# Kernel optimization log

Hardware: AMD Instinct MI355X
Metric: run time of the kernel (lower is better)

## Reference

```python
import jax, jax.numpy as jnp
import numpy as np

N_EMBED = 384
HEAD_SIZE = 64
B, T = 128, 512


def rope(x):
    # Faithful to source: fres = 1/1000**(arange(0,dim,2)//dim) -> integer
    # floor-div makes the exponent all zeros, so fres == 1 everywhere.
    Bx, Tx, D = x.shape
    half = D // 2
    fres = jnp.ones((half,), dtype=jnp.float32)
    ang = jnp.arange(Tx, dtype=jnp.float32)[:, None] * fres[None, :]  # (T, half)
    cos, sin = jnp.cos(ang), jnp.sin(ang)
    xr = x.reshape(Bx, Tx, half, 2)
    xe, xo = xr[..., 0], xr[..., 1]
    oe = xe * cos - xo * sin
    oo = xe * sin + xo * cos
    return jnp.stack([oe, oo], axis=-1).reshape(Bx, Tx, D)


def setup_inputs() -> dict:
    key = jax.random.key(0)
    ks = jax.random.split(key, 7)
    s = 1.0 / np.sqrt(N_EMBED)
    return {
        "x": jax.random.normal(ks[0], (B, T, N_EMBED), dtype=jnp.float32),
        "wq": jax.random.uniform(ks[1], (N_EMBED, HEAD_SIZE), jnp.float32, -s, s),
        "bq": jax.random.uniform(ks[2], (HEAD_SIZE,), jnp.float32, -s, s),
        "wk": jax.random.uniform(ks[3], (N_EMBED, HEAD_SIZE), jnp.float32, -s, s),
        "bk": jax.random.uniform(ks[4], (HEAD_SIZE,), jnp.float32, -s, s),
        "wv": jax.random.uniform(ks[5], (N_EMBED, HEAD_SIZE), jnp.float32, -s, s),
        "bv": jax.random.uniform(ks[6], (HEAD_SIZE,), jnp.float32, -s, s),
    }


def reference(x, wq, bq, wk, bk, wv, bv):
    Bx, Tx, C = x.shape  # C = n_embed; scale uses C per the source (not head_size)
    q = rope(x @ wq + bq)
    k = rope(x @ wk + bk)
    wei = jnp.einsum("bqd,bkd->bqk", q, k) * (C ** -0.5)  # (B, T, T)
    causal = jnp.tril(jnp.ones((Tx, Tx), dtype=bool))
    wei = jnp.where(causal, wei, -jnp.inf)
    wei = jax.nn.softmax(wei, axis=-1)
    v = x @ wv + bv
    return jnp.einsum("bqk,bkd->bqd", wei, v)
```

## Files before the change

kernel.cpp:

```cpp
#include <hip/hip_runtime.h>

#define TSEQ 512
#define NB   128
#define CDIM 384
#define HD   64
#define QSCALE 0.051031036307982884f
#define MBIAS  8.0f

typedef _Float16 half8  __attribute__((ext_vector_type(8)));
typedef _Float16 half4  __attribute__((ext_vector_type(4)));
typedef float    floatx4 __attribute__((ext_vector_type(4)));

__global__ void prep_w(const float* __restrict__ wq, const float* __restrict__ wk,
                       const float* __restrict__ wv, _Float16* __restrict__ Wt)
{
    int i = blockIdx.x * 256 + threadIdx.x;
    const int per = CDIM * HD;
    if (i >= 3 * per) return;
    int mat = i / per;
    int rem = i - mat * per;
    int k = rem / HD;
    int n = rem - k * HD;
    const float* w = (mat == 0) ? wq : ((mat == 1) ? wk : wv);
    Wt[((size_t)mat * HD + n) * CDIM + k] = (_Float16)w[rem];
}

__global__ __launch_bounds__(256) void qkv_gemm(
    const float* __restrict__ x, const _Float16* __restrict__ Wt,
    const float* __restrict__ bq, const float* __restrict__ bk,
    const float* __restrict__ bv,
    _Float16* __restrict__ Qw, _Float16* __restrict__ Kw,
    _Float16* __restrict__ Vtw, int b0)
{
    const int tid  = threadIdx.x;
    const int wave = tid >> 6;
    const int lane = tid & 63;
    const int l16  = lane & 15;
    const int quad = lane >> 4;

    const int row0 = blockIdx.x * 64;

    const float* xp = x + ((size_t)(b0 * TSEQ + row0) + l16) * CDIM + quad * 8;
    const _Float16* wp = Wt + (size_t)(wave * 16 + l16) * CDIM + quad * 8;

    floatx4 acc[12];
#pragma unroll
    for (int i = 0; i < 12; ++i)
#pragma unroll
        for (int r = 0; r < 4; ++r) acc[i][r] = 0.f;

    floatx4 ar[4][2];
    half8   br[3];
#pragma unroll
    for (int rt = 0; rt < 4; ++rt) {
        const float* p = xp + (size_t)rt * 16 * CDIM;
        ar[rt][0] = *(const floatx4*)p;
        ar[rt][1] = *(const floatx4*)(p + 4);
    }
#pragma unroll
    for (int m = 0; m < 3; ++m)
        br[m] = *(const half8*)(wp + (size_t)m * 64 * CDIM);

#pragma unroll
    for (int s = 0; s < 12; ++s) {
        floatx4 nr[4][2];
        half8   nb[3];
        if (s < 11) {
            const int kn = (s + 1) * 32;
#pragma unroll
            for (int rt = 0; rt < 4; ++rt) {
                const float* p = xp + (size_t)rt * 16 * CDIM + kn;
                nr[rt][0] = *(const floatx4*)p;
                nr[rt][1] = *(const floatx4*)(p + 4);
            }
#pragma unroll
            for (int m = 0; m < 3; ++m)
                nb[m] = *(const half8*)(wp + (size_t)m * 64 * CDIM + kn);
        }
        half8 a[4];
#pragma unroll
        for (int rt = 0; rt < 4; ++rt)
#pragma unroll
            for (int jj = 0; jj < 8; ++jj)
                a[rt][jj] = (_Float16)(jj < 4 ? ar[rt][0][jj] : ar[rt][1][jj - 4]);
#pragma unroll
        for (int m = 0; m < 3; ++m)
#pragma unroll
            for (int rt = 0; rt < 4; ++rt)
                acc[m * 4 + rt] =
                    __builtin_amdgcn_mfma_f32_16x16x32_f16(a[rt], br[m], acc[m * 4 + rt], 0, 0, 0);
        if (s < 11) {
#pragma unroll
            for (int rt = 0; rt < 4; ++rt) { ar[rt][0] = nr[rt][0]; ar[rt][1] = nr[rt][1]; }
#pragma unroll
            for (int m = 0; m < 3; ++m) br[m] = nb[m];
        }
    }

    const int c = wave * 16 + l16;
    const float bqv = bq[c], bkv = bk[c], bvv = bv[c];
    const int bidx = row0 >> 9;
    const int t00  = row0 & (TSEQ - 1);

#pragma unroll
    for (int rt = 0; rt < 4; ++rt) {
        half4 vpack;
#pragma unroll
        for (int r = 0; r < 4; ++r) {
            const int tr = t00 + rt * 16 + quad * 4 + r;
            const float st = sinf((float)tr);
            const float ct = cosf((float)tr);
            const int row = row0 + rt * 16 + quad * 4 + r;
            float vq = acc[rt][r] + bqv;
            float pq = __shfl_xor(vq, 1);
            vq = (c & 1) ? (pq * st + vq * ct) : (vq * ct - pq * st);
            Qw[(size_t)row * HD + c] = (_Float16)(vq * QSCALE);
            float vk = acc[4 + rt][r] + bkv;
            float pk = __shfl_xor(vk, 1);
            vk = (c & 1) ? (pk * st + vk * ct) : (vk * ct - pk * st);
            Kw[(size_t)row * HD + c] = (_Float16)vk;
            vpack[r] = (_Float16)(acc[8 + rt][r] + bvv);
        }
        const int tl0 = t00 + rt * 16 + quad * 4;
        *(half4*)(Vtw + ((size_t)bidx * HD + c) * TSEQ + tl0) = vpack;
    }
}

__global__ __launch_bounds__(256) void attn_kernel(
    const _Float16* __restrict__ Qw, const _Float16* __restrict__ Kw,
    const _Float16* __restrict__ Vtw, float* __restrict__ out, int b0)
{
    const int bl   = blockIdx.x;
    const int qt   = blockIdx.y;
    const int tid  = threadIdx.x;
    const int wave = tid >> 6;
    const int lane = tid & 63;
    const int l16  = lane & 15;
    const int quad = lane >> 4;

    __shared__ __align__(16) _Float16 pbuf[4][16][72];

    const _Float16* Qb = Qw  + (size_t)bl * TSEQ * HD;
    const _Float16* Kb = Kw  + (size_t)bl * TSEQ * HD;
    const _Float16* Vb = Vtw + (size_t)bl * HD * TSEQ;

    const int qr0 = qt * 64 + wave * 16;

    half8 aQ0 = *(const half8*)(Qb + (size_t)(qr0 + l16) * HD + quad * 8);
    half8 aQ1 = *(const half8*)(Qb + (size_t)(qr0 + l16) * HD + 32 + quad * 8);

    half8 ones;
#pragma unroll
    for (int jj = 0; jj < 8; ++jj) ones[jj] = (_Float16)1.f;

    floatx4 accO[4], accL;
#pragma unroll
    for (int s4 = 0; s4 < 4; ++s4)
#pragma unroll
        for (int r = 0; r < 4; ++r) accO[s4][r] = 0.f;
#pragma unroll
    for (int r = 0; r < 4; ++r) accL[r] = 0.f;

    for (int j = 0; j <= qt; ++j) {
        const int kb = j * 64;

        floatx4 st4[4];
#pragma unroll
        for (int s4 = 0; s4 < 4; ++s4) {
#pragma unroll
            for (int r = 0; r < 4; ++r) st4[s4][r] = 0.f;
            const _Float16* kp = Kb + (size_t)(kb + s4 * 16 + l16) * HD + quad * 8;
            half8 bK0 = *(const half8*)(kp);
            half8 bK1 = *(const half8*)(kp + 32);
            st4[s4] = __builtin_amdgcn_mfma_f32_16x16x32_f16(bK0, aQ0, st4[s4], 0, 0, 0);
            st4[s4] = __builtin_amdgcn_mfma_f32_16x16x32_f16(bK1, aQ1, st4[s4], 0, 0, 0);
        }

        half8 bV0[4], bV1[4];
#pragma unroll
        for (int s4 = 0; s4 < 4; ++s4) {
            const _Float16* vp = Vb + (size_t)(s4 * 16 + l16) * TSEQ + kb + quad * 8;
            bV0[s4] = *(const half8*)(vp);
            bV1[s4] = *(const half8*)(vp + 32);
        }

        const int qrow = qr0 + l16;
        if (j == qt) {
#pragma unroll
            for (int s4 = 0; s4 < 4; ++s4) {
                half4 w;
#pragma unroll
                for (int r = 0; r < 4; ++r) {
                    const int kcol = kb + s4 * 16 + quad * 4 + r;
                    float p = __expf(fminf(st4[s4][r], 18.f) - MBIAS);
                    w[r] = (_Float16)((kcol > qrow) ? 0.f : p);
                }
                *(half4*)(&pbuf[wave][l16][s4 * 16 + quad * 4]) = w;
            }
        } else {
#pragma unroll
            for (int s4 = 0; s4 < 4; ++s4) {
                half4 w;
#pragma unroll
                for (int r = 0; r < 4; ++r)
                    w[r] = (_Float16)__expf(fminf(st4[s4][r], 18.f) - MBIAS);
                *(half4*)(&pbuf[wave][l16][s4 * 16 + quad * 4]) = w;
            }
        }

        half8 aP0 = *(const half8*)(&pbuf[wave][l16][quad * 8]);
        half8 aP1 = *(const half8*)(&pbuf[wave][l16][32 + quad * 8]);

#pragma unroll
        for (int s4 = 0; s4 < 4; ++s4) {
            accO[s4] = __builtin_amdgcn_mfma_f32_16x16x32_f16(aP0, bV0[s4], accO[s4], 0, 0, 0);
            accO[s4] = __builtin_amdgcn_mfma_f32_16x16x32_f16(aP1, bV1[s4], accO[s4], 0, 0, 0);
        }
        accL = __builtin_amdgcn_mfma_f32_16x16x32_f16(aP0, ones, accL, 0, 0, 0);
        accL = __builtin_amdgcn_mfma_f32_16x16x32_f16(aP1, ones, accL, 0, 0, 0);
    }

    float inv[4];
#pragma unroll
    for (int r = 0; r < 4; ++r) inv[r] = 1.f / accL[r];
#pragma unroll
    for (int s4 = 0; s4 < 4; ++s4) {
        const int dcol = s4 * 16 + l16;
#pragma unroll
        for (int r = 0; r < 4; ++r) {
            const int qr = qr0 + quad * 4 + r;
            out[((size_t)(b0 + bl) * TSEQ + qr) * HD + dcol] = accO[s4][r] * inv[r];
        }
    }
}

extern "C" void kernel_launch(void* const* d_in, const int* in_sizes, int n_in,
                              void* d_out, int out_size, void* d_ws, size_t ws_size,
                              hipStream_t stream)
{
    char* ws = (char*)d_ws;
    _Float16* Wt = (_Float16*)ws;
    char* qkv_base = ws + 147456;

    const size_t per_b = (size_t)3 * TSEQ * HD * sizeof(_Float16);
    size_t avail = (ws_size > (size_t)147456) ? ws_size - 147456 : per_b;
    int nbc = (int)(avail / per_b);
    if (nbc > NB) nbc = NB;
    if (nbc < 1)  nbc = 1;

    const size_t chunk_elems = (size_t)nbc * TSEQ * HD;
    _Float16* Qw  = (_Float16*)qkv_base;
    _Float16* Kw  = Qw + chunk_elems;
    _Float16* Vtw = Kw + chunk_elems;

    prep_w<<<dim3((3 * CDIM * HD + 255) / 256), dim3(256), 0, stream>>>(
        (const float*)d_in[1], (const float*)d_in[3], (const float*)d_in[5], Wt);

    for (int b0 = 0; b0 < NB; b0 += nbc) {
        const int nb = (NB - b0 < nbc) ? (NB - b0) : nbc;
        qkv_gemm<<<dim3(nb * 8), dim3(256), 0, stream>>>(
            (const float*)d_in[0], Wt, (const float*)d_in[2], (const float*)d_in[4],
            (const float*)d_in[6], Qw, Kw, Vtw, b0);
        attn_kernel<<<dim3(nb, 8), dim3(256), 0, stream>>>(
            Qw, Kw, Vtw, (float*)d_out, b0);
    }
}
```

Before: 255.2 us.

## Stage QKV GEMM tiles in LDS and share K/V loads across two query tiles

```diff
diff --git a/kernel.cpp b/kernel.cpp
--- a/kernel.cpp
+++ b/kernel.cpp
@@ -10,6 +10,13 @@
 typedef _Float16 half8  __attribute__((ext_vector_type(8)));
 typedef _Float16 half4  __attribute__((ext_vector_type(4)));
 typedef float    floatx4 __attribute__((ext_vector_type(4)));
+
+typedef __attribute__((address_space(3))) unsigned int lds_u32;
+typedef const __attribute__((address_space(1))) unsigned int g_u32;
+
+__device__ __forceinline__ void load_lds16(const void* g, void* l) {
+    __builtin_amdgcn_global_load_lds((g_u32*)g, (lds_u32*)l, 16, 0, 0);
+}
 
 __global__ void prep_w(const float* __restrict__ wq, const float* __restrict__ wk,
                        const float* __restrict__ wv, _Float16* __restrict__ Wt)
@@ -32,6 +39,9 @@
     _Float16* __restrict__ Qw, _Float16* __restrict__ Kw,
     _Float16* __restrict__ Vtw, int b0)
 {
+    __shared__ __align__(16) float    xs[8 * 64 * 8];
+    __shared__ __align__(16) _Float16 wsb[8 * 192 * 8];
+
     const int tid  = threadIdx.x;
     const int wave = tid >> 6;
     const int lane = tid & 63;
@@ -39,9 +49,7 @@
     const int quad = lane >> 4;
 
     const int row0 = blockIdx.x * 64;
-
-    const float* xp = x + ((size_t)(b0 * TSEQ + row0) + l16) * CDIM + quad * 8;
-    const _Float16* wp = Wt + (size_t)(wave * 16 + l16) * CDIM + quad * 8;
+    const size_t rowg = (size_t)b0 * TSEQ + row0;
 
     floatx4 acc[12];
 #pragma unroll
@@ -49,80 +57,86 @@
 #pragma unroll
         for (int r = 0; r < 4; ++r) acc[i][r] = 0.f;
 
-    floatx4 ar[4][2];
-    half8   br[3];
-#pragma unroll
-    for (int rt = 0; rt < 4; ++rt) {
-        const float* p = xp + (size_t)rt * 16 * CDIM;
-        ar[rt][0] = *(const floatx4*)p;
-        ar[rt][1] = *(const floatx4*)(p + 4);
-    }
-#pragma unroll
-    for (int m = 0; m < 3; ++m)
-        br[m] = *(const half8*)(wp + (size_t)m * 64 * CDIM);
-
-#pragma unroll
-    for (int s = 0; s < 12; ++s) {
-        floatx4 nr[4][2];
-        half8   nb[3];
-        if (s < 11) {
-            const int kn = (s + 1) * 32;
-#pragma unroll
-            for (int rt = 0; rt < 4; ++rt) {
-                const float* p = xp + (size_t)rt * 16 * CDIM + kn;
-                nr[rt][0] = *(const floatx4*)p;
-                nr[rt][1] = *(const floatx4*)(p + 4);
-            }
-#pragma unroll
-            for (int m = 0; m < 3; ++m)
-                nb[m] = *(const half8*)(wp + (size_t)m * 64 * CDIM + kn);
-        }
-        half8 a[4];
-#pragma unroll
-        for (int rt = 0; rt < 4; ++rt)
+    for (int c = 0; c < 6; ++c) {
+        const int kk0 = c * 64;
+
+#pragma unroll
+        for (int i = 0; i < 4; ++i) {
+            const int I    = wave * 4 + i;
+            const int cell = I * 32 + (lane >> 1);
+            const int kblk = cell >> 6;
+            const int m    = cell & 63;
+            const int kin0 = (lane & 1) * 4;
+            const float* src = x + (rowg + m) * CDIM + kk0 + kblk * 8 + kin0;
+            load_lds16(src, (char*)xs + I * 1024);
+        }
+#pragma unroll
+        for (int i = 0; i < 6; ++i) {
+            const int I2   = wave * 6 + i;
+            const int c2   = I2 * 64 + lane;
+            const int kblk = c2 / 192;
+            const int n    = c2 - kblk * 192;
+            const _Float16* src = Wt + (size_t)n * CDIM + kk0 + kblk * 8;
+            load_lds16(src, (char*)wsb + I2 * 1024);
+        }
+        __syncthreads();
+
+#pragma unroll
+        for (int kb2 = 0; kb2 < 2; ++kb2) {
+            const int kblk = kb2 * 4 + quad;
+            const float* ap = xs + ((size_t)kblk * 64 + wave * 16 + l16) * 8;
+            floatx4 a0 = *(const floatx4*)ap;
+            floatx4 a1 = *(const floatx4*)(ap + 4);
+            half8 a;
 #pragma unroll
             for (int jj = 0; jj < 8; ++jj)
-                a[rt][jj] = (_Float16)(jj < 4 ? ar[rt][0][jj] : ar[rt][1][jj - 4]);
-#pragma unroll
-        for (int m = 0; m < 3; ++m)
-#pragma unroll
-            for (int rt = 0; rt < 4; ++rt)
-                acc[m * 4 + rt] =
-                    __builtin_amdgcn_mfma_f32_16x16x32_f16(a[rt], br[m], acc[m * 4 + rt], 0, 0, 0);
-        if (s < 11) {
-#pragma unroll
-            for (int rt = 0; rt < 4; ++rt) { ar[rt][0] = nr[rt][0]; ar[rt][1] = nr[rt][1]; }
-#pragma unroll
-            for (int m = 0; m < 3; ++m) br[m] = nb[m];
-        }
-    }
-
-    const int c = wave * 16 + l16;
-    const float bqv = bq[c], bkv = bk[c], bvv = bv[c];
+                a[jj] = (_Float16)(jj < 4 ? a0[jj] : a1[jj - 4]);
+            const _Float16* bp = wsb + ((size_t)kblk * 192 + l16) * 8;
+#pragma unroll
+            for (int i = 0; i < 12; ++i) {
+                half8 bb = *(const half8*)(bp + i * 128);
+                acc[i] = __builtin_amdgcn_mfma_f32_16x16x32_f16(a, bb, acc[i], 0, 0, 0);
+            }
+        }
+        __syncthreads();
+    }
+
+    float bq4[4], bk4[4], bv4[4];
+#pragma unroll
+    for (int s4 = 0; s4 < 4; ++s4) {
+        const int cc = s4 * 16 + l16;
+        bq4[s4] = bq[cc]; bk4[s4] = bk[cc]; bv4[s4] = bv[cc];
+    }
+    const int t00  = (row0 & (TSEQ - 1)) + wave * 16 + quad * 4;
     const int bidx = row0 >> 9;
-    const int t00  = row0 & (TSEQ - 1);
-
-#pragma unroll
-    for (int rt = 0; rt < 4; ++rt) {
+    const int rowb = row0 + wave * 16 + quad * 4;
+
+#pragma unroll
+    for (int r = 0; r < 4; ++r) {
+        const int t = t00 + r;
+        const float st = sinf((float)t);
+        const float ct = cosf((float)t);
+        const int row = rowb + r;
+#pragma unroll
+        for (int s4 = 0; s4 < 4; ++s4) {
+            const int cc = s4 * 16 + l16;
+            float vq = acc[s4][r] + bq4[s4];
+            float pq = __shfl_xor(vq, 1);
+            vq = (cc & 1) ? (pq * st + vq * ct) : (vq * ct - pq * st);
+            Qw[(size_t)row * HD + cc] = (_Float16)(vq * QSCALE);
+            float vk = acc[4 + s4][r] + bk4[s4];
+            float pk = __shfl_xor(vk, 1);
+            vk = (cc & 1) ? (pk * st + vk * ct) : (vk * ct - pk * st);
+            Kw[(size_t)row * HD + cc] = (_Float16)vk;
+        }
+    }
+#pragma unroll
+    for (int s4 = 0; s4 < 4; ++s4) {
+        const int cc = s4 * 16 + l16;
         half4 vpack;
 #pragma unroll
-        for (int r = 0; r < 4; ++r) {
-            const int tr = t00 + rt * 16 + quad * 4 + r;
-            const float st = sinf((float)tr);
-            const float ct = cosf((float)tr);
-            const int row = row0 + rt * 16 + quad * 4 + r;
-            float vq = acc[rt][r] + bqv;
-            float pq = __shfl_xor(vq, 1);
-            vq = (c & 1) ? (pq * st + vq * ct) : (vq * ct - pq * st);
-            Qw[(size_t)row * HD + c] = (_Float16)(vq * QSCALE);
-            float vk = acc[4 + rt][r] + bkv;
-            float pk = __shfl_xor(vk, 1);
-            vk = (c & 1) ? (pk * st + vk * ct) : (vk * ct - pk * st);
-            Kw[(size_t)row * HD + c] = (_Float16)vk;
-            vpack[r] = (_Float16)(acc[8 + rt][r] + bvv);
-        }
-        const int tl0 = t00 + rt * 16 + quad * 4;
-        *(half4*)(Vtw + ((size_t)bidx * HD + c) * TSEQ + tl0) = vpack;
+        for (int r = 0; r < 4; ++r) vpack[r] = (_Float16)(acc[8 + s4][r] + bv4[s4]);
+        *(half4*)(Vtw + ((size_t)bidx * HD + cc) * TSEQ + t00) = vpack;
     }
 }
 
@@ -130,8 +144,8 @@
     const _Float16* __restrict__ Qw, const _Float16* __restrict__ Kw,
     const _Float16* __restrict__ Vtw, float* __restrict__ out, int b0)
 {
-    const int bl   = blockIdx.x;
-    const int qt   = blockIdx.y;
+    const int qt   = blockIdx.x;
+    const int bl   = blockIdx.y;
     const int tid  = threadIdx.x;
     const int wave = tid >> 6;
     const int lane = tid & 63;
@@ -144,92 +158,129 @@
     const _Float16* Kb = Kw  + (size_t)bl * TSEQ * HD;
     const _Float16* Vb = Vtw + (size_t)bl * HD * TSEQ;
 
-    const int qr0 = qt * 64 + wave * 16;
-
-    half8 aQ0 = *(const half8*)(Qb + (size_t)(qr0 + l16) * HD + quad * 8);
-    half8 aQ1 = *(const half8*)(Qb + (size_t)(qr0 + l16) * HD + 32 + quad * 8);
+    const int qA = qt * 128 + wave * 16;
+    const int qB = qA + 64;
+    const int jd = 2 * qt;
+
+    half8 aQA0 = *(const half8*)(Qb + (size_t)(qA + l16) * HD + quad * 8);
+    half8 aQA1 = *(const half8*)(Qb + (size_t)(qA + l16) * HD + 32 + quad * 8);
+    half8 aQB0 = *(const half8*)(Qb + (size_t)(qB + l16) * HD + quad * 8);
+    half8 aQB1 = *(const half8*)(Qb + (size_t)(qB + l16) * HD + 32 + quad * 8);
 
     half8 ones;
 #pragma unroll
     for (int jj = 0; jj < 8; ++jj) ones[jj] = (_Float16)1.f;
 
-    floatx4 accO[4], accL;
-#pragma unroll
-    for (int s4 = 0; s4 < 4; ++s4)
-#pragma unroll
-        for (int r = 0; r < 4; ++r) accO[s4][r] = 0.f;
-#pragma unroll
-    for (int r = 0; r < 4; ++r) accL[r] = 0.f;
-
-    for (int j = 0; j <= qt; ++j) {
+    floatx4 accO[8], accL[2];
+#pragma unroll
+    for (int i = 0; i < 8; ++i)
+#pragma unroll
+        for (int r = 0; r < 4; ++r) accO[i][r] = 0.f;
+#pragma unroll
+    for (int s = 0; s < 2; ++s)
+#pragma unroll
+        for (int r = 0; r < 4; ++r) accL[s][r] = 0.f;
+
+    for (int j = 0; j <= jd + 1; ++j) {
         const int kb = j * 64;
 
-        floatx4 st4[4];
+        half8 bK0[4], bK1[4], bV0[4], bV1[4];
 #pragma unroll
         for (int s4 = 0; s4 < 4; ++s4) {
-#pragma unroll
-            for (int r = 0; r < 4; ++r) st4[s4][r] = 0.f;
             const _Float16* kp = Kb + (size_t)(kb + s4 * 16 + l16) * HD + quad * 8;
-            half8 bK0 = *(const half8*)(kp);
-            half8 bK1 = *(const half8*)(kp + 32);
-            st4[s4] = __builtin_amdgcn_mfma_f32_16x16x32_f16(bK0, aQ0, st4[s4], 0, 0, 0);
-            st4[s4] = __builtin_amdgcn_mfma_f32_16x16x32_f16(bK1, aQ1, st4[s4], 0, 0, 0);
-        }
-
-        half8 bV0[4], bV1[4];
-#pragma unroll
-        for (int s4 = 0; s4 < 4; ++s4) {
+            bK0[s4] = *(const half8*)(kp);
+            bK1[s4] = *(const half8*)(kp + 32);
             const _Float16* vp = Vb + (size_t)(s4 * 16 + l16) * TSEQ + kb + quad * 8;
             bV0[s4] = *(const half8*)(vp);
             bV1[s4] = *(const half8*)(vp + 32);
         }
 
-        const int qrow = qr0 + l16;
-        if (j == qt) {
+        if (j <= jd) {
+            floatx4 st4[4];
+#pragma unroll
+            for (int s4 = 0; s4 < 4; ++s4) {
+#pragma unroll
+                for (int r = 0; r < 4; ++r) st4[s4][r] = 0.f;
+                st4[s4] = __builtin_amdgcn_mfma_f32_16x16x32_f16(bK0[s4], aQA0, st4[s4], 0, 0, 0);
+                st4[s4] = __builtin_amdgcn_mfma_f32_16x16x32_f16(bK1[s4], aQA1, st4[s4], 0, 0, 0);
+            }
+            const int qrow = qA + l16;
 #pragma unroll
             for (int s4 = 0; s4 < 4; ++s4) {
                 half4 w;
 #pragma unroll
                 for (int r = 0; r < 4; ++r) {
-                    const int kcol = kb + s4 * 16 + quad * 4 + r;
                     float p = __expf(fminf(st4[s4][r], 18.f) - MBIAS);
-                    w[r] = (_Float16)((kcol > qrow) ? 0.f : p);
+                    if (j == jd) {
+                        const int kcol = kb + s4 * 16 + quad * 4 + r;
+                        if (kcol > qrow) p = 0.f;
+                    }
+                    w[r] = (_Float16)p;
                 }
                 *(half4*)(&pbuf[wave][l16][s4 * 16 + quad * 4]) = w;
             }
-        } else {
+            half8 aP0 = *(const half8*)(&pbuf[wave][l16][quad * 8]);
+            half8 aP1 = *(const half8*)(&pbuf[wave][l16][32 + quad * 8]);
+#pragma unroll
+            for (int s4 = 0; s4 < 4; ++s4) {
+                accO[s4] = __builtin_amdgcn_mfma_f32_16x16x32_f16(aP0, bV0[s4], accO[s4], 0, 0, 0);
+                accO[s4] = __builtin_amdgcn_mfma_f32_16x16x32_f16(aP1, bV1[s4], accO[s4], 0, 0, 0);
+            }
+            accL[0] = __builtin_amdgcn_mfma_f32_16x16x32_f16(aP0, ones, accL[0], 0, 0, 0);
+            accL[0] = __builtin_amdgcn_mfma_f32_16x16x32_f16(aP1, ones, accL[0], 0, 0, 0);
+        }
+
+        {
+            floatx4 st4[4];
+#pragma unroll
+            for (int s4 = 0; s4 < 4; ++s4) {
+#pragma unroll
+                for (int r = 0; r < 4; ++r) st4[s4][r] = 0.f;
+                st4[s4] = __builtin_amdgcn_mfma_f32_16x16x32_f16(bK0[s4], aQB0, st4[s4], 0, 0, 0);
+                st4[s4] = __builtin_amdgcn_mfma_f32_16x16x32_f16(bK1[s4], aQB1, st4[s4], 0, 0, 0);
+            }
+            const int qrow = qB + l16;
 #pragma unroll
             for (int s4 = 0; s4 < 4; ++s4) {
                 half4 w;
 #pragma unroll
-                for (int r = 0; r < 4; ++r)
-                    w[r] = (_Float16)__expf(fminf(st4[s4][r], 18.f) - MBIAS);
+                for (int r = 0; r < 4; ++r) {
+                    float p = __expf(fminf(st4[s4][r], 18.f) - MBIAS);
+                    if (j == jd + 1) {
+                        const int kcol = kb + s4 * 16 + quad * 4 + r;
+                        if (kcol > qrow) p = 0.f;
+                    }
+                    w[r] = (_Float16)p;
+                }
                 *(half4*)(&pbuf[wave][l16][s4 * 16 + quad * 4]) = w;
             }
-        }
-
-        half8 aP0 = *(const half8*)(&pbuf[wave][l16][quad * 8]);
-        half8 aP1 = *(const half8*)(&pbuf[wave][l16][32 + quad * 8]);
-
+            half8 aP0 = *(const half8*)(&pbuf[wave][l16][quad * 8]);
+            half8 aP1 = *(const half8*)(&pbuf[wave][l16][32 + quad * 8]);
+#pragma unroll
+            for (int s4 = 0; s4 < 4; ++s4) {
+                accO[4 + s4] = __builtin_amdgcn_mfma_f32_16x16x32_f16(aP0, bV0[s4], accO[4 + s4], 0, 0, 0);
+                accO[4 + s4] = __builtin_amdgcn_mfma_f32_16x16x32_f16(aP1, bV1[s4], accO[4 + s4], 0, 0, 0);
+            }
+            accL[1] = __builtin_amdgcn_mfma_f32_16x16x32_f16(aP0, ones, accL[1], 0, 0, 0);
+            accL[1] = __builtin_amdgcn_mfma_f32_16x16x32_f16(aP1, ones, accL[1], 0, 0, 0);
+        }
+    }
+
+#pragma unroll
+    for (int s = 0; s < 2; ++s) {
+        const int qbase = (s == 0) ? qA : qB;
+        float inv[4];
+#pragma unroll
+        for (int r = 0; r < 4; ++r) inv[r] = 1.f / accL[s][r];
 #pragma unroll
         for (int s4 = 0; s4 < 4; ++s4) {
-            accO[s4] = __builtin_amdgcn_mfma_f32_16x16x32_f16(aP0, bV0[s4], accO[s4], 0, 0, 0);
-            accO[s4] = __builtin_amdgcn_mfma_f32_16x16x32_f16(aP1, bV1[s4], accO[s4], 0, 0, 0);
-        }
-        accL = __builtin_amdgcn_mfma_f32_16x16x32_f16(aP0, ones, accL, 0, 0, 0);
-        accL = __builtin_amdgcn_mfma_f32_16x16x32_f16(aP1, ones, accL, 0, 0, 0);
-    }
-
-    float inv[4];
-#pragma unroll
-    for (int r = 0; r < 4; ++r) inv[r] = 1.f / accL[r];
-#pragma unroll
-    for (int s4 = 0; s4 < 4; ++s4) {
-        const int dcol = s4 * 16 + l16;
-#pragma unroll
-        for (int r = 0; r < 4; ++r) {
-            const int qr = qr0 + quad * 4 + r;
-            out[((size_t)(b0 + bl) * TSEQ + qr) * HD + dcol] = accO[s4][r] * inv[r];
+            const int dcol = s4 * 16 + l16;
+#pragma unroll
+            for (int r = 0; r < 4; ++r) {
+                const int qr = qbase + quad * 4 + r;
+                out[((size_t)(b0 + bl) * TSEQ + qr) * HD + dcol] =
+                    accO[s * 4 + s4][r] * inv[r];
+            }
         }
     }
 }
@@ -261,7 +312,7 @@
         qkv_gemm<<<dim3(nb * 8), dim3(256), 0, stream>>>(
             (const float*)d_in[0], Wt, (const float*)d_in[2], (const float*)d_in[4],
             (const float*)d_in[6], Qw, Kw, Vtw, b0);
-        attn_kernel<<<dim3(nb, 8), dim3(256), 0, stream>>>(
+        attn_kernel<<<dim3(4, nb), dim3(256), 0, stream>>>(
             Qw, Kw, Vtw, (float*)d_out, b0);
     }
 }
```

After: 212.9 us. -16.6%, faster.
